# Kernel optimization log

Measured on AMD Instinct MI355X. Metric: run time of the kernel, lower is better.

## Reference

```python
import jax, jax.numpy as jnp
import numpy as np

FP8_MAX = 448.0  # torch.finfo(float8_e4m3fn).max
BLK = 128
EPS = 1e-12

def fp8_round(x):
    # saturated cast to float8_e4m3fn and back (emulates to_fp8_saturated)
    y = jnp.clip(x, -FP8_MAX, FP8_MAX)
    return y.astype(jnp.float8_e4m3fn).astype(jnp.float32)

def per_tile_quant_dequant(x):
    # activation: 1x128 tiles along the feature dim
    S, D = x.shape
    t = x.reshape(S, D // BLK, BLK)
    amax = jnp.max(jnp.abs(t), axis=-1, keepdims=True)
    scale = jnp.maximum(amax, EPS) / FP8_MAX
    q = fp8_round(t / scale)
    return (q * scale).reshape(S, D)

def per_block_quant_dequant_weight(w):
    # weight: 128x128 blocks, w is [ne, dout, din]
    ne, do, di = w.shape
    blk = w.reshape(ne, do // BLK, BLK, di // BLK, BLK)
    amax = jnp.max(jnp.abs(blk), axis=(2, 4), keepdims=True)
    scale = jnp.maximum(amax, EPS) / FP8_MAX
    q = fp8_round(blk / scale)
    return (q * scale).reshape(ne, do, di)

def setup_inputs() -> dict:
    key = jax.random.key(0)
    k1, k2 = jax.random.split(key)
    NE, DOUT, DIN, SEQ = 8, 1024, 2048, 16384
    x = jax.random.normal(k1, (SEQ, DIN), dtype=jnp.float32)
    w = jax.random.normal(k2, (NE * DOUT, DIN), dtype=jnp.float32) * 0.02
    tokens_per_expert = jnp.full((NE,), SEQ // NE, dtype=jnp.int32)
    return {"input": x, "tokens_per_expert": tokens_per_expert, "weight": w}

def reference(input, tokens_per_expert, weight):
    NE = tokens_per_expert.shape[0]
    S, DIN = input.shape
    DOUT = weight.shape[0] // NE
    w = weight.reshape(NE, DOUT, DIN)
    w_dq = per_block_quant_dequant_weight(w)   # fp8 per-block weight, dequantized
    x_dq = per_tile_quant_dequant(input)       # fp8 per-tile activation, dequantized
    # grouped varlen GEMM; tokens are split equally across experts here
    T = S // NE
    xe = x_dq.reshape(NE, T, DIN)
    out = jnp.einsum('etd,eod->eto', xe, w_dq)  # [ne, T, dout]
    return out.reshape(S, DOUT)
```

## Files before the change

kernel.cpp:

```cpp
#include <hip/hip_runtime.h>
#include <hip/hip_bf16.h>
#include <hip/hip_fp8.h>

#define SEQ   16384
#define DIN_  2048
#define DOUT_ 1024
#define NE_   8
#define TPE   (SEQ / NE_)
#define NT    (DIN_ / 64)

typedef __bf16 bf16x8 __attribute__((ext_vector_type(8)));
typedef __bf16 bf16x4 __attribute__((ext_vector_type(4)));
typedef float  f32x4  __attribute__((ext_vector_type(4)));

#define GLD(gp, lp) __builtin_amdgcn_global_load_lds( \
    (const __attribute__((address_space(1))) unsigned int*)(gp), \
    (__attribute__((address_space(3))) unsigned int*)(lp), 16, 0, 0)

__device__ __forceinline__ float fp8_round_dq_m(float v, float sinv, float s) {
    float r = v * sinv;
    r = fminf(fmaxf(r, -448.0f), 448.0f);
    __hip_fp8_e4m3 q(r);
    return (float)q * s;
}

__global__ __launch_bounds__(256) void quant_x_kernel(const float* __restrict__ X,
                                                      __bf16* __restrict__ Xq) {
    const int t    = threadIdx.x;
    const int lane = t & 63;
    const int wave = t >> 6;
    const int tile = wave * 4 + (lane >> 4);
    const int sub  = lane & 15;
    const size_t off = (size_t)tile * 128 + sub * 8;

    const int row0 = blockIdx.x * 2;
    const float* pa = X + (size_t)row0 * DIN_ + off;
    const float* pb = X + (size_t)(row0 + 1) * DIN_ + off;

    float4 a0 = *(const float4*)pa;
    float4 a1 = *(const float4*)(pa + 4);
    float4 b0 = *(const float4*)pb;
    float4 b1 = *(const float4*)(pb + 4);

    float ma = fmaxf(fmaxf(fmaxf(fabsf(a0.x), fabsf(a0.y)), fmaxf(fabsf(a0.z), fabsf(a0.w))),
                     fmaxf(fmaxf(fabsf(a1.x), fabsf(a1.y)), fmaxf(fabsf(a1.z), fabsf(a1.w))));
    float mb = fmaxf(fmaxf(fmaxf(fabsf(b0.x), fabsf(b0.y)), fmaxf(fabsf(b0.z), fabsf(b0.w))),
                     fmaxf(fmaxf(fabsf(b1.x), fabsf(b1.y)), fmaxf(fabsf(b1.z), fabsf(b1.w))));
    #pragma unroll
    for (int off2 = 1; off2 < 16; off2 <<= 1) {
        ma = fmaxf(ma, __shfl_xor(ma, off2, 64));
        mb = fmaxf(mb, __shfl_xor(mb, off2, 64));
    }

    const float sa = fmaxf(ma, 1e-12f) / 448.0f, sia = 1.0f / sa;
    const float sb = fmaxf(mb, 1e-12f) / 448.0f, sib = 1.0f / sb;

    bf16x8 oa, ob;
    oa[0] = (__bf16)fp8_round_dq_m(a0.x, sia, sa);
    oa[1] = (__bf16)fp8_round_dq_m(a0.y, sia, sa);
    oa[2] = (__bf16)fp8_round_dq_m(a0.z, sia, sa);
    oa[3] = (__bf16)fp8_round_dq_m(a0.w, sia, sa);
    oa[4] = (__bf16)fp8_round_dq_m(a1.x, sia, sa);
    oa[5] = (__bf16)fp8_round_dq_m(a1.y, sia, sa);
    oa[6] = (__bf16)fp8_round_dq_m(a1.z, sia, sa);
    oa[7] = (__bf16)fp8_round_dq_m(a1.w, sia, sa);
    ob[0] = (__bf16)fp8_round_dq_m(b0.x, sib, sb);
    ob[1] = (__bf16)fp8_round_dq_m(b0.y, sib, sb);
    ob[2] = (__bf16)fp8_round_dq_m(b0.z, sib, sb);
    ob[3] = (__bf16)fp8_round_dq_m(b0.w, sib, sb);
    ob[4] = (__bf16)fp8_round_dq_m(b1.x, sib, sb);
    ob[5] = (__bf16)fp8_round_dq_m(b1.y, sib, sb);
    ob[6] = (__bf16)fp8_round_dq_m(b1.z, sib, sb);
    ob[7] = (__bf16)fp8_round_dq_m(b1.w, sib, sb);
    *(bf16x8*)(Xq + (size_t)row0 * DIN_ + off) = oa;
    *(bf16x8*)(Xq + (size_t)(row0 + 1) * DIN_ + off) = ob;
}

__global__ __launch_bounds__(256) void quant_w_kernel(const float* __restrict__ W,
                                                      __bf16* __restrict__ Wq) {
    const int rb = blockIdx.x >> 4;
    const int cb = blockIdx.x & 15;
    const int t  = threadIdx.x;

    const float* base = W + (size_t)(rb * 128) * DIN_ + cb * 128;
    const int r0 = t >> 5;
    const int c0 = (t & 31) * 4;

    float4 v[16];
    float m = 0.0f;
    #pragma unroll
    for (int i = 0; i < 16; ++i) {
        v[i] = *(const float4*)(base + (size_t)(i * 8 + r0) * DIN_ + c0);
        m = fmaxf(m, fmaxf(fmaxf(fabsf(v[i].x), fabsf(v[i].y)),
                           fmaxf(fabsf(v[i].z), fabsf(v[i].w))));
    }
    #pragma unroll
    for (int off = 1; off < 64; off <<= 1)
        m = fmaxf(m, __shfl_xor(m, off, 64));
    __shared__ float smx[4];
    if ((t & 63) == 0) smx[t >> 6] = m;
    __syncthreads();
    const float amax = fmaxf(fmaxf(smx[0], smx[1]), fmaxf(smx[2], smx[3]));
    const float s    = fmaxf(amax, 1e-12f) / 448.0f;
    const float sinv = 1.0f / s;

    __bf16* obase = Wq + (size_t)(rb * 128) * DIN_ + cb * 128;
    #pragma unroll
    for (int i = 0; i < 16; ++i) {
        bf16x4 o;
        o[0] = (__bf16)fp8_round_dq_m(v[i].x, sinv, s);
        o[1] = (__bf16)fp8_round_dq_m(v[i].y, sinv, s);
        o[2] = (__bf16)fp8_round_dq_m(v[i].z, sinv, s);
        o[3] = (__bf16)fp8_round_dq_m(v[i].w, sinv, s);
        *(bf16x4*)(obase + (size_t)(i * 8 + r0) * DIN_ + c0) = o;
    }
}

__global__ __launch_bounds__(512, 2) void gemm_kernel(const __bf16* __restrict__ X,
                                                      const __bf16* __restrict__ W,
                                                      float* __restrict__ out) {
    __shared__ __align__(16) unsigned char lds[131072];

    const int bid  = blockIdx.x;
    const int wgid = (bid & 7) * 32 + (bid >> 3);
    const int e    = wgid >> 5;
    const int tile = wgid & 31;
    const int brow = tile >> 2;
    const int bcol = tile & 3;

    const int t     = threadIdx.x;
    const int lane  = t & 63;
    const int wave  = t >> 6;
    const int wm    = wave >> 2;
    const int wn    = wave & 3;
    const int flane = lane & 15;

    const __bf16* Xt = X + (size_t)(e * TPE + brow * 256) * DIN_;
    const __bf16* Wt = W + (size_t)(e * DOUT_ + bcol * 256) * DIN_;

    auto stage_part = [&](int H) {
        if (H >= 4 * NT) return;
        const int k2   = H >> 2;
        const int r    = H & 3;
        const bool isB = (r < 2);
        const int half = r & 1;
        const int buf  = k2 & 1;
        const __bf16* src = isB ? Wt : Xt;
        const unsigned base = (isB ? 65536u : 0u) + (unsigned)buf * 32768u
                            + (unsigned)half * 16384u;
        #pragma unroll
        for (int i = 0; i < 2; ++i) {
            const unsigned p = (unsigned)i * 8192u + (unsigned)t * 16u;
            const unsigned q = p ^ (((p >> 7) & 7u) << 4);
            GLD(src + (size_t)(half * 128 + (q >> 7)) * DIN_ + k2 * 64 + ((q & 127u) >> 1),
                &lds[base + p]);
        }
    };

    auto ld_frag = [&](unsigned base, int row, int kh) -> bf16x8 {
        unsigned p = (unsigned)row * 128u + (unsigned)kh * 64u + (unsigned)(lane >> 4) * 16u;
        p ^= ((p >> 7) & 7u) << 4;
        return *(const bf16x8*)&lds[base + p];
    };

    f32x4 acc[8][4] = {};

    stage_part(0); stage_part(1); stage_part(2); stage_part(3);
    stage_part(4); stage_part(5); stage_part(6);
    asm volatile("s_waitcnt vmcnt(6)" ::: "memory");
    __builtin_amdgcn_s_barrier();

    for (int kt = 0; kt < NT; ++kt) {
        const int buf = kt & 1;
        const unsigned Ab = (unsigned)buf * 32768u;
        const unsigned Bb = 65536u + (unsigned)buf * 32768u;
        const int H0 = 4 * kt + 7;

        bf16x8 b0[4], b1[4], a[4];

        #pragma unroll
        for (int n = 0; n < 4; ++n) b0[n] = ld_frag(Bb, wn * 64 + n * 16 + flane, 0);
        #pragma unroll
        for (int m = 0; m < 4; ++m) a[m] = ld_frag(Ab, wm * 128 + m * 16 + flane, 0);
        stage_part(H0);
        __builtin_amdgcn_s_barrier();
        asm volatile("s_waitcnt lgkmcnt(0)" ::: "memory");
        __builtin_amdgcn_sched_barrier(0);
        __builtin_amdgcn_s_setprio(1);
        #pragma unroll
        for (int m = 0; m < 4; ++m)
            #pragma unroll
            for (int n = 0; n < 4; ++n)
                acc[m][n] = __builtin_amdgcn_mfma_f32_16x16x32_bf16(a[m], b0[n], acc[m][n], 0, 0, 0);
        __builtin_amdgcn_s_setprio(0);
        __builtin_amdgcn_s_barrier();

        #pragma unroll
        for (int n = 0; n < 4; ++n) b1[n] = ld_frag(Bb, wn * 64 + n * 16 + flane, 1);
        #pragma unroll
        for (int m = 0; m < 4; ++m) a[m] = ld_frag(Ab, wm * 128 + m * 16 + flane, 1);
        stage_part(H0 + 1);
        __builtin_amdgcn_s_barrier();
        asm volatile("s_waitcnt lgkmcnt(0)" ::: "memory");
        __builtin_amdgcn_sched_barrier(0);
        __builtin_amdgcn_s_setprio(1);
        #pragma unroll
        for (int m = 0; m < 4; ++m)
            #pragma unroll
            for (int n = 0; n < 4; ++n)
                acc[m][n] = __builtin_amdgcn_mfma_f32_16x16x32_bf16(a[m], b1[n], acc[m][n], 0, 0, 0);
        __builtin_amdgcn_s_setprio(0);
        __builtin_amdgcn_s_barrier();

        #pragma unroll
        for (int m = 0; m < 4; ++m) a[m] = ld_frag(Ab, wm * 128 + (m + 4) * 16 + flane, 0);
        stage_part(H0 + 2);
        __builtin_amdgcn_s_barrier();
        asm volatile("s_waitcnt lgkmcnt(0)" ::: "memory");
        __builtin_amdgcn_sched_barrier(0);
        __builtin_amdgcn_s_setprio(1);
        #pragma unroll
        for (int m = 0; m < 4; ++m)
            #pragma unroll
            for (int n = 0; n < 4; ++n)
                acc[m + 4][n] = __builtin_amdgcn_mfma_f32_16x16x32_bf16(a[m], b0[n], acc[m + 4][n], 0, 0, 0);
        __builtin_amdgcn_s_setprio(0);
        __builtin_amdgcn_s_barrier();

        #pragma unroll
        for (int m = 0; m < 4; ++m) a[m] = ld_frag(Ab, wm * 128 + (m + 4) * 16 + flane, 1);
        stage_part(H0 + 3);
        __builtin_amdgcn_s_barrier();
        asm volatile("s_waitcnt lgkmcnt(0)" ::: "memory");
        __builtin_amdgcn_sched_barrier(0);
        __builtin_amdgcn_s_setprio(1);
        #pragma unroll
        for (int m = 0; m < 4; ++m)
            #pragma unroll
            for (int n = 0; n < 4; ++n)
                acc[m + 4][n] = __builtin_amdgcn_mfma_f32_16x16x32_bf16(a[m], b1[n], acc[m + 4][n], 0, 0, 0);
        __builtin_amdgcn_s_setprio(0);
        if (kt < NT - 2) {
            asm volatile("s_waitcnt vmcnt(6)" ::: "memory");
        } else {
            asm volatile("s_waitcnt vmcnt(0)" ::: "memory");
        }
        __builtin_amdgcn_s_barrier();
    }

    const int orow0 = e * TPE + brow * 256 + wm * 128;
    const int ocol0 = bcol * 256 + wn * 64;
    const int rl = (lane >> 4) * 4;
    const int cl = lane & 15;
    #pragma unroll
    for (int m = 0; m < 8; ++m)
        #pragma unroll
        for (int n = 0; n < 4; ++n)
            #pragma unroll
            for (int j = 0; j < 4; ++j) {
                const int r = orow0 + m * 16 + rl + j;
                const int c = ocol0 + n * 16 + cl;
                out[(size_t)r * DOUT_ + c] = acc[m][n][j];
            }
}

extern "C" void kernel_launch(void* const* d_in, const int* in_sizes, int n_in,
                              void* d_out, int out_size, void* d_ws, size_t ws_size,
                              hipStream_t stream) {
    const float* x = (const float*)d_in[0];
    const float* w = (const float*)d_in[2];
    float* out = (float*)d_out;

    __bf16* xq = (__bf16*)d_ws;
    __bf16* wq = (__bf16*)((char*)d_ws + (size_t)SEQ * DIN_ * sizeof(__bf16));

    quant_x_kernel<<<SEQ / 2, 256, 0, stream>>>(x, xq);
    quant_w_kernel<<<(NE_ * DOUT_ / 128) * (DIN_ / 128), 256, 0, stream>>>(w, wq);
    gemm_kernel<<<NE_ * (TPE / 256) * (DOUT_ / 256), 512, 0, stream>>>(xq, wq, out);
}
```

Baseline: 121.1 us.

## Software-pipeline LDS fragment loads across MFMA phases with split-K-half LDS layout

Restructures the GEMM main loop so LDS fragment reads for the next MFMA phase are issued before the current phase and overlap with it, using double register sets (aA/aB) and partial lgkmcnt waits. The LDS layout changes to separate 32-wide K halves (64-byte rows) without XOR swizzle, and global-to-LDS staging is reordered and retimed with new vmcnt thresholds. This aims to hide LDS latency and cut barrier stalls, but unswizzled 64-byte rows may cause LDS bank conflicts, and register pressure rises.

```diff
diff --git a/kernel.cpp b/kernel.cpp
--- a/kernel.cpp
+++ b/kernel.cpp
@@ -138,113 +138,93 @@
     const __bf16* Xt = X + (size_t)(e * TPE + brow * 256) * DIN_;
     const __bf16* Wt = W + (size_t)(e * DOUT_ + bcol * 256) * DIN_;
 
-    auto stage_part = [&](int H) {
-        if (H >= 4 * NT) return;
-        const int k2   = H >> 2;
-        const int r    = H & 3;
-        const bool isB = (r < 2);
-        const int half = r & 1;
-        const int buf  = k2 & 1;
-        const __bf16* src = isB ? Wt : Xt;
-        const unsigned base = (isB ? 65536u : 0u) + (unsigned)buf * 32768u
-                            + (unsigned)half * 16384u;
+    auto stage = [&](int j, bool isA, int kh) {
+        if (j >= NT) return;
+        const int buf = j & 1;
+        const unsigned base = (isA ? 0u : 65536u) + (unsigned)(buf * 2 + kh) * 16384u;
+        const __bf16* src = isA ? Xt : Wt;
+        const int col = j * 64 + kh * 32 + (t & 3) * 8;
         #pragma unroll
         for (int i = 0; i < 2; ++i) {
             const unsigned p = (unsigned)i * 8192u + (unsigned)t * 16u;
-            const unsigned q = p ^ (((p >> 7) & 7u) << 4);
-            GLD(src + (size_t)(half * 128 + (q >> 7)) * DIN_ + k2 * 64 + ((q & 127u) >> 1),
-                &lds[base + p]);
+            GLD(src + (size_t)(p >> 6) * DIN_ + col, &lds[base + p]);
         }
     };
 
-    auto ld_frag = [&](unsigned base, int row, int kh) -> bf16x8 {
-        unsigned p = (unsigned)row * 128u + (unsigned)kh * 64u + (unsigned)(lane >> 4) * 16u;
-        p ^= ((p >> 7) & 7u) << 4;
-        return *(const bf16x8*)&lds[base + p];
+    auto ldf = [&](unsigned base, int row) -> bf16x8 {
+        return *(const bf16x8*)&lds[base + (unsigned)row * 64u + (unsigned)(lane >> 4) * 16u];
     };
 
+    bf16x8 aA[4], aB[4], b0[4], b1[4];
     f32x4 acc[8][4] = {};
 
-    stage_part(0); stage_part(1); stage_part(2); stage_part(3);
-    stage_part(4); stage_part(5); stage_part(6);
-    asm volatile("s_waitcnt vmcnt(6)" ::: "memory");
+    #define ABASE(buf, kh) ((unsigned)((buf) * 2 + (kh)) * 16384u)
+    #define BBASE(buf, kh) (65536u + (unsigned)((buf) * 2 + (kh)) * 16384u)
+    #define PRE_A(dst, buf, kh, m0) \
+        { _Pragma("unroll") for (int m_ = 0; m_ < 4; ++m_) \
+            dst[m_] = ldf(ABASE(buf, kh), wm * 128 + ((m0) + m_) * 16 + flane); }
+    #define PRE_B(dst, buf, kh) \
+        { _Pragma("unroll") for (int n_ = 0; n_ < 4; ++n_) \
+            dst[n_] = ldf(BBASE(buf, kh), wn * 64 + n_ * 16 + flane); }
+    #define MFMA4x4(alo, aset, bset) \
+        { _Pragma("unroll") for (int m_ = 0; m_ < 4; ++m_) \
+            _Pragma("unroll") for (int n_ = 0; n_ < 4; ++n_) \
+                acc[(alo) + m_][n_] = __builtin_amdgcn_mfma_f32_16x16x32_bf16( \
+                    aset[m_], bset[n_], acc[(alo) + m_][n_], 0, 0, 0); }
+
+    stage(0, false, 0); stage(0, false, 1); stage(0, true, 0);
+    stage(0, true, 1);  stage(1, false, 0); stage(1, false, 1); stage(1, true, 0);
+    asm volatile("s_waitcnt vmcnt(8)" ::: "memory");
     __builtin_amdgcn_s_barrier();
+    PRE_A(aA, 0, 0, 0);
+    PRE_B(b0, 0, 0);
 
     for (int kt = 0; kt < NT; ++kt) {
         const int buf = kt & 1;
-        const unsigned Ab = (unsigned)buf * 32768u;
-        const unsigned Bb = 65536u + (unsigned)buf * 32768u;
-        const int H0 = 4 * kt + 7;
-
-        bf16x8 b0[4], b1[4], a[4];
-
-        #pragma unroll
-        for (int n = 0; n < 4; ++n) b0[n] = ld_frag(Bb, wn * 64 + n * 16 + flane, 0);
-        #pragma unroll
-        for (int m = 0; m < 4; ++m) a[m] = ld_frag(Ab, wm * 128 + m * 16 + flane, 0);
-        stage_part(H0);
-        __builtin_amdgcn_s_barrier();
-        asm volatile("s_waitcnt lgkmcnt(0)" ::: "memory");
-        __builtin_amdgcn_sched_barrier(0);
-        __builtin_amdgcn_s_setprio(1);
-        #pragma unroll
-        for (int m = 0; m < 4; ++m)
-            #pragma unroll
-            for (int n = 0; n < 4; ++n)
-                acc[m][n] = __builtin_amdgcn_mfma_f32_16x16x32_bf16(a[m], b0[n], acc[m][n], 0, 0, 0);
-        __builtin_amdgcn_s_setprio(0);
-        __builtin_amdgcn_s_barrier();
-
-        #pragma unroll
-        for (int n = 0; n < 4; ++n) b1[n] = ld_frag(Bb, wn * 64 + n * 16 + flane, 1);
-        #pragma unroll
-        for (int m = 0; m < 4; ++m) a[m] = ld_frag(Ab, wm * 128 + m * 16 + flane, 1);
-        stage_part(H0 + 1);
-        __builtin_amdgcn_s_barrier();
-        asm volatile("s_waitcnt lgkmcnt(0)" ::: "memory");
-        __builtin_amdgcn_sched_barrier(0);
-        __builtin_amdgcn_s_setprio(1);
-        #pragma unroll
-        for (int m = 0; m < 4; ++m)
-            #pragma unroll
-            for (int n = 0; n < 4; ++n)
-                acc[m][n] = __builtin_amdgcn_mfma_f32_16x16x32_bf16(a[m], b1[n], acc[m][n], 0, 0, 0);
-        __builtin_amdgcn_s_setprio(0);
-        __builtin_amdgcn_s_barrier();
-
-        #pragma unroll
-        for (int m = 0; m < 4; ++m) a[m] = ld_frag(Ab, wm * 128 + (m + 4) * 16 + flane, 0);
-        stage_part(H0 + 2);
-        __builtin_amdgcn_s_barrier();
-        asm volatile("s_waitcnt lgkmcnt(0)" ::: "memory");
-        __builtin_amdgcn_sched_barrier(0);
-        __builtin_amdgcn_s_setprio(1);
-        #pragma unroll
-        for (int m = 0; m < 4; ++m)
-            #pragma unroll
-            for (int n = 0; n < 4; ++n)
-                acc[m + 4][n] = __builtin_amdgcn_mfma_f32_16x16x32_bf16(a[m], b0[n], acc[m + 4][n], 0, 0, 0);
-        __builtin_amdgcn_s_setprio(0);
-        __builtin_amdgcn_s_barrier();
-
-        #pragma unroll
-        for (int m = 0; m < 4; ++m) a[m] = ld_frag(Ab, wm * 128 + (m + 4) * 16 + flane, 1);
-        stage_part(H0 + 3);
-        __builtin_amdgcn_s_barrier();
-        asm volatile("s_waitcnt lgkmcnt(0)" ::: "memory");
-        __builtin_amdgcn_sched_barrier(0);
-        __builtin_amdgcn_s_setprio(1);
-        #pragma unroll
-        for (int m = 0; m < 4; ++m)
-            #pragma unroll
-            for (int n = 0; n < 4; ++n)
-                acc[m + 4][n] = __builtin_amdgcn_mfma_f32_16x16x32_bf16(a[m], b1[n], acc[m + 4][n], 0, 0, 0);
-        __builtin_amdgcn_s_setprio(0);
-        if (kt < NT - 2) {
-            asm volatile("s_waitcnt vmcnt(6)" ::: "memory");
-        } else {
-            asm volatile("s_waitcnt vmcnt(0)" ::: "memory");
+
+        PRE_A(aB, buf, 0, 4);
+        stage(kt + 1, true, 1);
+        asm volatile("s_waitcnt lgkmcnt(4)" ::: "memory");
+        __builtin_amdgcn_sched_barrier(0);
+        __builtin_amdgcn_s_setprio(1);
+        MFMA4x4(0, aA, b0);
+        __builtin_amdgcn_s_setprio(0);
+        if (kt < NT - 1) asm volatile("s_waitcnt vmcnt(8)" ::: "memory");
+        else             asm volatile("s_waitcnt vmcnt(0)" ::: "memory");
+        __builtin_amdgcn_s_barrier();
+
+        PRE_A(aA, buf, 1, 0);
+        PRE_B(b1, buf, 1);
+        stage(kt + 2, false, 0);
+        asm volatile("s_waitcnt lgkmcnt(8)" ::: "memory");
+        __builtin_amdgcn_sched_barrier(0);
+        __builtin_amdgcn_s_setprio(1);
+        MFMA4x4(4, aB, b0);
+        __builtin_amdgcn_s_setprio(0);
+        __builtin_amdgcn_s_barrier();
+
+        PRE_A(aB, buf, 1, 4);
+        asm volatile("s_waitcnt lgkmcnt(4)" ::: "memory");
+        __builtin_amdgcn_sched_barrier(0);
+        __builtin_amdgcn_s_setprio(1);
+        MFMA4x4(0, aA, b1);
+        __builtin_amdgcn_s_setprio(0);
+        if (kt < NT - 2)      asm volatile("s_waitcnt vmcnt(4)" ::: "memory");
+        else if (kt == NT - 2) asm volatile("s_waitcnt vmcnt(2)" ::: "memory");
+        __builtin_amdgcn_s_barrier();
+
+        if (kt < NT - 1) {
+            PRE_A(aA, buf ^ 1, 0, 0);
+            PRE_B(b0, buf ^ 1, 0);
         }
+        stage(kt + 2, false, 1);
+        stage(kt + 2, true, 0);
+        if (kt < NT - 1) asm volatile("s_waitcnt lgkmcnt(8)" ::: "memory");
+        else             asm volatile("s_waitcnt lgkmcnt(0)" ::: "memory");
+        __builtin_amdgcn_sched_barrier(0);
+        __builtin_amdgcn_s_setprio(1);
+        MFMA4x4(4, aB, b1);
+        __builtin_amdgcn_s_setprio(0);
         __builtin_amdgcn_s_barrier();
     }
 
```

After: 122.0 us. Within noise of the previous version (+0.7%).
